# Optimization experiments

Hardware: AMD Instinct MI355X
Metric: run time of the kernel (lower is better)

Reference implementation:

```python
import jax, jax.numpy as jnp
import numpy as np

D_MODEL = 1024
D_HEAD = 64
B, S = 4, 4096


def setup_inputs() -> dict:
    key = jax.random.key(0)
    ks = jax.random.split(key, 7)
    inv = 1.0 / np.sqrt(D_MODEL)
    return {
        "x": jax.random.normal(ks[0], (B, S, D_MODEL), dtype=jnp.float32),
        "W_q": jax.random.normal(ks[1], (D_MODEL, D_HEAD), dtype=jnp.float32) * inv,
        "b_q": jax.random.normal(ks[2], (D_HEAD,), dtype=jnp.float32) * 0.02,
        "W_k": jax.random.normal(ks[3], (D_MODEL, D_HEAD), dtype=jnp.float32) * inv,
        "b_k": jax.random.normal(ks[4], (D_HEAD,), dtype=jnp.float32) * 0.02,
        "W_v": jax.random.normal(ks[5], (D_MODEL, D_HEAD), dtype=jnp.float32) * inv,
        "b_v": jax.random.normal(ks[6], (D_HEAD,), dtype=jnp.float32) * 0.02,
    }


def reference(x, W_q, b_q, W_k, b_k, W_v, b_v):
    # Projections: [B, S, d_head]
    Q = jnp.einsum("bsd,dh->bsh", x, W_q) + b_q
    K = jnp.einsum("bsd,dh->bsh", x, W_k) + b_k
    V = jnp.einsum("bsd,dh->bsh", x, W_v) + b_v
    scale = 1.0 / jnp.sqrt(jnp.asarray(Q.shape[-1], dtype=Q.dtype))
    scores = jnp.einsum("bqh,bkh->bqk", Q, K) * scale  # [B, S, S]
    seq_len = x.shape[1]
    causal = jnp.tril(jnp.ones((seq_len, seq_len), dtype=bool))
    scores = jnp.where(causal, scores, jnp.asarray(-jnp.inf, dtype=scores.dtype))
    A = jax.nn.softmax(scores, axis=-1)
    return jnp.einsum("bqk,bkh->bqh", A, V)  # [B, S, d_head]
```

## Files before the change

### kernel.cpp

```cpp
#include <hip/hip_runtime.h>

typedef __attribute__((ext_vector_type(4))) float f32x4;
typedef __attribute__((ext_vector_type(8))) short short8;
typedef unsigned short ushort_t;

constexpr int DM = 1024, DH = 64, S = 4096, B = 4;
constexpr float QSCALE = 0.125f * 1.44269504088896340736f;
constexpr int SPLIT = 4;

constexpr size_t WBT_OFF = 0;
constexpr size_t QB_OFF  = 393216;
constexpr size_t KB_OFF  = QB_OFF + 2097152;
constexpr size_t VT_OFF  = KB_OFF + 2097152;
constexpr size_t ML_OFF  = VT_OFF + 2097152;
constexpr size_t PO_OFF  = ML_OFF + 524288;

__device__ __forceinline__ ushort_t f2bf(float f) {
    unsigned u = __float_as_uint(f);
    u += 0x7FFFu + ((u >> 16) & 1u);
    return (ushort_t)(u >> 16);
}

__device__ __forceinline__ void gl_lds16(const void* g, void* l) {
    __builtin_amdgcn_global_load_lds(
        (const __attribute__((address_space(1))) unsigned int*)g,
        (__attribute__((address_space(3))) unsigned int*)l, 16, 0, 0);
}

__global__ __launch_bounds__(256) void prep_w_kernel(
    const float* __restrict__ Wq, const float* __restrict__ Wk,
    const float* __restrict__ Wv, ushort_t* __restrict__ wbt)
{
    const int n = blockIdx.x;
    const int p = n >> 6, d = n & 63;
    const float* W = (p == 0) ? Wq : (p == 1) ? Wk : Wv;
    const int k0 = threadIdx.x * 4;
    ushort4 pack;
    pack.x = f2bf(W[(k0 + 0) * DH + d]);
    pack.y = f2bf(W[(k0 + 1) * DH + d]);
    pack.z = f2bf(W[(k0 + 2) * DH + d]);
    pack.w = f2bf(W[(k0 + 3) * DH + d]);
    *reinterpret_cast<ushort4*>(wbt + (size_t)n * DM + k0) = pack;
}

__global__ __launch_bounds__(512, 4) void qkv_mfma_kernel(
    const float* __restrict__ x, const ushort_t* __restrict__ wbt,
    const float* __restrict__ bq, const float* __restrict__ bk,
    const float* __restrict__ bv,
    ushort_t* __restrict__ qb, ushort_t* __restrict__ kb, ushort_t* __restrict__ vt)
{
    __shared__ ushort_t As[2][32][32];
    __shared__ uint4 BsU[2][768];

    const int tid = threadIdx.x;
    const int wid = tid >> 6, lane = tid & 63;
    const int q16 = lane & 15, lg = lane >> 4;
    const int sub = wid & 1, np = wid >> 1;
    const int r0 = blockIdx.x * 32;
    const char* wB = (const char*)wbt;

    const int ar = tid >> 4;
    const int ak = (tid & 15) * 2;
    const float* xrow = x + (size_t)(r0 + ar) * DM + ak;

    auto writeA = [&](int buf, float2 a) {
        const unsigned pk = (unsigned)f2bf(a.x) | ((unsigned)f2bf(a.y) << 16);
        *reinterpret_cast<unsigned*>((char*)&As[buf][0][0] + ar * 64 + ak * 2) = pk;
    };
    auto stageB = [&](int buf, int kk) {
        {
            const int sg = wid;
            gl_lds16(wB + (size_t)(sg * 16 + (lane >> 2)) * 2048 + kk * 2
                        + ((((lane & 3) ^ ((lane >> 2) & 3))) << 4),
                     (char*)&BsU[buf][0] + sg * 1024 + lane * 16);
        }
        if (wid < 4) {
            const int sg = wid + 8;
            gl_lds16(wB + (size_t)(sg * 16 + (lane >> 2)) * 2048 + kk * 2
                        + ((((lane & 3) ^ ((lane >> 2) & 3))) << 4),
                     (char*)&BsU[buf][0] + sg * 1024 + lane * 16);
        }
    };

    f32x4 acc[3];
#pragma unroll
    for (int j = 0; j < 3; ++j) acc[j] = {0.f, 0.f, 0.f, 0.f};

    {
        const float2 a0 = *(const float2*)(xrow + 0);
        stageB(0, 0);
        writeA(0, a0);
    }
    __syncthreads();

    const int arow = sub * 16 + q16;
    for (int s = 0; s < 32; ++s) {
        const int buf = s & 1;
        float2 aP;
        if (s + 1 < 32) {
            aP = *(const float2*)(xrow + (s + 1) * 32);
            stageB(buf ^ 1, (s + 1) * 32);
        }
        const short8 Af = *reinterpret_cast<const short8*>(
            (const char*)&As[buf][0][0] + arow * 64 + lg * 16);
        __builtin_amdgcn_s_setprio(1);
#pragma unroll
        for (int j = 0; j < 3; ++j) {
            const int nt = np * 3 + j;
            const short8 Bf = *(const short8*)(
                (const char*)&BsU[buf][0] + (nt * 16 + q16) * 64 + ((lg ^ (q16 & 3)) << 4));
            acc[j] = __builtin_amdgcn_mfma_f32_16x16x32_bf16(Af, Bf, acc[j], 0, 0, 0);
        }
        __builtin_amdgcn_s_setprio(0);
        if (s + 1 < 32) writeA(buf ^ 1, aP);
        __syncthreads();
    }

#pragma unroll
    for (int j = 0; j < 3; ++j) {
        const int nt = np * 3 + j;
        const int p = nt >> 2, d = ((nt & 3) << 4) + q16;
        const float* bp = (p == 0) ? bq : (p == 1) ? bk : bv;
        const float bb = bp[d];
#pragma unroll
        for (int r = 0; r < 4; ++r) {
            const int m = r0 + sub * 16 + (lg << 2) + r;
            const float v = acc[j][r] + bb;
            if (p == 0) {
                qb[(size_t)m * 64 + d] = f2bf(v * QSCALE);
            } else if (p == 1) {
                kb[(size_t)m * 64 + d] = f2bf(v);
            } else {
                const int bb_ = m >> 12, sx = m & 4095;
                vt[(size_t)bb_ * 262144 + (size_t)d * 4096 + sx] = f2bf(v);
            }
        }
    }
}

__global__ __launch_bounds__(256, 4) void attn_mfma_kernel(
    const ushort_t* __restrict__ qb, const ushort_t* __restrict__ kb,
    const ushort_t* __restrict__ vt, ushort_t* __restrict__ po,
    float* __restrict__ ml)
{
    __shared__ uint4 LsU[2][2048];
    __shared__ uint4 PsU[4][256];

    const int tid = threadIdx.x;
    const int wid = tid >> 6, lane = tid & 63;
    const int q16 = lane & 15, lg = lane >> 4;
    const int z = blockIdx.y;

    const int linear = blockIdx.x;
    const int xcd = linear & 7, idx = linear >> 3;
    const int b = xcd >> 1;
    const int qt = 63 - (idx * 2 + (xcd & 1));

    const int qrow = qt * 64 + wid * 16 + q16;
    const ushort_t* Qb = qb + (size_t)b * S * 64;
    const char* KbB = (const char*)(kb + (size_t)b * S * 64);
    const char* VtB = (const char*)(vt + (size_t)b * 64 * S);

    const short8 qf0 = *(const short8*)(Qb + (size_t)qrow * 64 + lg * 8);
    const short8 qf1 = *(const short8*)(Qb + (size_t)qrow * 64 + 32 + lg * 8);

    f32x4 o[4];
#pragma unroll
    for (int nt = 0; nt < 4; ++nt) o[nt] = {0.f, 0.f, 0.f, 0.f};
    float m = -1e30f, l = 0.f;

    char* PsC = (char*)&PsU[wid][0];
    const int ntiles = (qt >> 1) + 1;

    auto stage = [&](int t, int buf) {
        const int kv0 = t * 128;
#pragma unroll
        for (int i = 0; i < 8; ++i) {
            const int slot = i * 256 + tid;
            char* dst = (char*)&LsU[buf][0] + slot * 16;
            if (slot < 1024) {
                const int row = slot >> 3, ch = slot & 7;
                gl_lds16(KbB + (size_t)(kv0 + row) * 128 + ((ch ^ (row & 7)) << 4), dst);
            } else {
                const int s2 = slot - 1024;
                const int d = s2 >> 4, ch = s2 & 15;
                gl_lds16(VtB + (size_t)d * (S * 2) + kv0 * 2 + ((ch ^ (d & 15)) << 4), dst);
            }
        }
    };

    int buf = 0;
    if (z < ntiles) stage(z, 0);
    __syncthreads();

    for (int t = z; t < ntiles; t += SPLIT) {
        if (t + SPLIT < ntiles) stage(t + SPLIT, buf ^ 1);
        const char* KsC = (const char*)&LsU[buf][0];
        const char* VsC = KsC + 16384;
        const int kv0 = t * 128;

        f32x4 st[8];
#pragma unroll
        for (int mt = 0; mt < 8; ++mt) st[mt] = {0.f, 0.f, 0.f, 0.f};
#pragma unroll
        for (int ks = 0; ks < 2; ++ks) {
#pragma unroll
            for (int mg = 0; mg < 2; ++mg) {
                short8 kf[4];
#pragma unroll
                for (int j = 0; j < 4; ++j) {
                    const int mt = mg * 4 + j;
                    kf[j] = *(const short8*)(
                        KsC + (mt * 16 + q16) * 128 + (((lg + 4 * ks) ^ (q16 & 7)) << 4));
                }
                __builtin_amdgcn_s_setprio(1);
#pragma unroll
                for (int j = 0; j < 4; ++j)
                    st[mg * 4 + j] = __builtin_amdgcn_mfma_f32_16x16x32_bf16(
                        kf[j], (ks ? qf1 : qf0), st[mg * 4 + j], 0, 0, 0);
                __builtin_amdgcn_s_setprio(0);
            }
        }

        if (t == ntiles - 1) {
#pragma unroll
            for (int mt = 0; mt < 8; ++mt)
#pragma unroll
                for (int r = 0; r < 4; ++r)
                    if (kv0 + mt * 16 + (lg << 2) + r > qrow) st[mt][r] = -1e30f;
        }

        float tm = -1e30f;
#pragma unroll
        for (int mt = 0; mt < 8; ++mt)
#pragma unroll
            for (int r = 0; r < 4; ++r) tm = fmaxf(tm, st[mt][r]);
        tm = fmaxf(tm, __shfl_xor(tm, 16));
        tm = fmaxf(tm, __shfl_xor(tm, 32));

        if (__all(tm <= m)) {
            float ps = 0.f;
#pragma unroll
            for (int mt = 0; mt < 8; ++mt)
#pragma unroll
                for (int r = 0; r < 4; ++r) {
                    const float pv = exp2f(st[mt][r] - m);
                    st[mt][r] = pv;
                    ps += pv;
                }
            ps += __shfl_xor(ps, 16);
            ps += __shfl_xor(ps, 32);
            l += ps;
        } else {
            const float mn = fmaxf(m, tm);
            const float corr = exp2f(m - mn);
            float ps = 0.f;
#pragma unroll
            for (int mt = 0; mt < 8; ++mt)
#pragma unroll
                for (int r = 0; r < 4; ++r) {
                    const float pv = exp2f(st[mt][r] - mn);
                    st[mt][r] = pv;
                    ps += pv;
                }
            ps += __shfl_xor(ps, 16);
            ps += __shfl_xor(ps, 32);
            l = l * corr + ps;
            m = mn;
            float corr_row[4];
#pragma unroll
            for (int r = 0; r < 4; ++r) corr_row[r] = __shfl(corr, (lg << 2) | r);
#pragma unroll
            for (int nt = 0; nt < 4; ++nt)
#pragma unroll
                for (int r = 0; r < 4; ++r) o[nt][r] *= corr_row[r];
        }

#pragma unroll
        for (int mt = 0; mt < 8; ++mt) {
            uint2 w;
            w.x = (unsigned)f2bf(st[mt][0]) | ((unsigned)f2bf(st[mt][1]) << 16);
            w.y = (unsigned)f2bf(st[mt][2]) | ((unsigned)f2bf(st[mt][3]) << 16);
            const int ch = (2 * mt + (lg >> 1)) ^ q16;
            *reinterpret_cast<uint2*>(PsC + q16 * 256 + ch * 16 + (lg & 1) * 8) = w;
        }

        __builtin_amdgcn_s_setprio(1);
#pragma unroll
        for (int ks = 0; ks < 4; ++ks) {
            const short8 pa = *reinterpret_cast<const short8*>(
                PsC + q16 * 256 + (((4 * ks + lg) ^ q16) << 4));
#pragma unroll
            for (int nt = 0; nt < 4; ++nt) {
                const short8 vf = *(const short8*)(
                    VsC + (nt * 16 + q16) * 256 + (((ks * 4 + lg) ^ q16) << 4));
                o[nt] = __builtin_amdgcn_mfma_f32_16x16x32_bf16(pa, vf, o[nt], 0, 0, 0);
            }
        }
        __builtin_amdgcn_s_setprio(0);

        __syncthreads();
        buf ^= 1;
    }

    const int rowbase = qt * 64 + wid * 16;
    const size_t zb = (size_t)z * B * S + (size_t)b * S;
#pragma unroll
    for (int nt = 0; nt < 4; ++nt)
#pragma unroll
        for (int r = 0; r < 4; ++r)
            po[(zb + rowbase + (lg << 2) + r) * 64 + nt * 16 + q16] = f2bf(o[nt][r]);
    if (lg == 0) {
        ml[(zb + rowbase + q16) * 2 + 0] = m;
        ml[(zb + rowbase + q16) * 2 + 1] = l;
    }
}

__global__ __launch_bounds__(256) void merge_kernel(
    const ushort_t* __restrict__ po, const float* __restrict__ ml,
    float* __restrict__ out)
{
    const int idx = blockIdx.x * 256 + threadIdx.x;
    const int row = idx >> 3, c8 = idx & 7;

    float mv[SPLIT], lv[SPLIT];
#pragma unroll
    for (int zz = 0; zz < SPLIT; ++zz) {
        const float2 t = *(const float2*)(ml + ((size_t)zz * B * S + row) * 2);
        mv[zz] = t.x; lv[zz] = t.y;
    }
    const float mm = fmaxf(fmaxf(mv[0], mv[1]), fmaxf(mv[2], mv[3]));
    float L = 0.f, cz[SPLIT];
#pragma unroll
    for (int zz = 0; zz < SPLIT; ++zz) { cz[zz] = exp2f(mv[zz] - mm); L += lv[zz] * cz[zz]; }
    const float inv = 1.0f / L;

    float acc[8];
#pragma unroll
    for (int e = 0; e < 8; ++e) acc[e] = 0.f;
#pragma unroll
    for (int zz = 0; zz < SPLIT; ++zz) {
        const uint4 pk = *(const uint4*)(po + ((size_t)zz * B * S + row) * 64 + c8 * 8);
        const unsigned w[4] = {pk.x, pk.y, pk.z, pk.w};
#pragma unroll
        for (int i = 0; i < 4; ++i) {
            acc[2 * i + 0] += cz[zz] * __uint_as_float((w[i] & 0xFFFFu) << 16);
            acc[2 * i + 1] += cz[zz] * __uint_as_float((w[i] >> 16) << 16);
        }
    }
    float4 o0 = make_float4(acc[0] * inv, acc[1] * inv, acc[2] * inv, acc[3] * inv);
    float4 o1 = make_float4(acc[4] * inv, acc[5] * inv, acc[6] * inv, acc[7] * inv);
    *(float4*)(out + (size_t)row * 64 + c8 * 8 + 0) = o0;
    *(float4*)(out + (size_t)row * 64 + c8 * 8 + 4) = o1;
}

extern "C" void kernel_launch(void* const* d_in, const int* in_sizes, int n_in,
                              void* d_out, int out_size, void* d_ws, size_t ws_size,
                              hipStream_t stream) {
    const float* x  = (const float*)d_in[0];
    const float* Wq = (const float*)d_in[1];
    const float* bq = (const float*)d_in[2];
    const float* Wk = (const float*)d_in[3];
    const float* bk = (const float*)d_in[4];
    const float* Wv = (const float*)d_in[5];
    const float* bv = (const float*)d_in[6];
    float* out = (float*)d_out;

    char* ws = (char*)d_ws;
    ushort_t* wbt = (ushort_t*)(ws + WBT_OFF);
    ushort_t* qbp = (ushort_t*)(ws + QB_OFF);
    ushort_t* kbp = (ushort_t*)(ws + KB_OFF);
    ushort_t* vtp = (ushort_t*)(ws + VT_OFF);
    float*    mlp = (float*)(ws + ML_OFF);
    ushort_t* pop = (ushort_t*)(ws + PO_OFF);

    hipLaunchKernelGGL(prep_w_kernel, dim3(192), dim3(256), 0, stream, Wq, Wk, Wv, wbt);
    hipLaunchKernelGGL(qkv_mfma_kernel, dim3(512), dim3(512), 0, stream,
                       x, wbt, bq, bk, bv, qbp, kbp, vtp);
    hipLaunchKernelGGL(attn_mfma_kernel, dim3(256, SPLIT), dim3(256), 0, stream,
                       qbp, kbp, vtp, pop, mlp);
    hipLaunchKernelGGL(merge_kernel, dim3(512), dim3(256), 0, stream, pop, mlp, out);
}
```

Before: 74.57 us.

## Load x directly into registers, quad-buffer weights, stream V from global

The QKV projection kernel drops the shared-memory A tile. Each lane now loads its x fragment straight from global one step ahead and converts it to bf16 in registers. The weight tiles become a 4-deep LDS ring with a vmcnt wait and one barrier per step, where there were two-stage buffers with a full syncthreads. The attention kernel stops staging V through LDS and instead loads V fragments directly from global into registers, double-buffered across the PV MFMA steps. This halves LDS use per block but lowers the launch-bounds occupancy hint from 4 to 3 and adds register pressure and uncoalesced global V reads.

```diff
diff --git a/kernel.cpp b/kernel.cpp
--- a/kernel.cpp
+++ b/kernel.cpp
@@ -49,8 +49,7 @@
     const float* __restrict__ bv,
     ushort_t* __restrict__ qb, ushort_t* __restrict__ kb, ushort_t* __restrict__ vt)
 {
-    __shared__ ushort_t As[2][32][32];
-    __shared__ uint4 BsU[2][768];
+    __shared__ uint4 BsU[4][768];
 
     const int tid = threadIdx.x;
     const int wid = tid >> 6, lane = tid & 63;
@@ -59,61 +58,56 @@
     const int r0 = blockIdx.x * 32;
     const char* wB = (const char*)wbt;
 
-    const int ar = tid >> 4;
-    const int ak = (tid & 15) * 2;
-    const float* xrow = x + (size_t)(r0 + ar) * DM + ak;
-
-    auto writeA = [&](int buf, float2 a) {
-        const unsigned pk = (unsigned)f2bf(a.x) | ((unsigned)f2bf(a.y) << 16);
-        *reinterpret_cast<unsigned*>((char*)&As[buf][0][0] + ar * 64 + ak * 2) = pk;
+    const float* xr = x + (size_t)(r0 + sub * 16 + q16) * DM + lg * 8;
+
+    const int sgA = wid, sgB = (wid & 3) + 8;
+    auto stageB = [&](int kk, int buf) {
+        gl_lds16(wB + (size_t)(sgA * 16 + (lane >> 2)) * 2048 + kk * 2
+                    + ((((lane & 3) ^ ((lane >> 2) & 3))) << 4),
+                 (char*)&BsU[buf][0] + sgA * 1024 + lane * 16);
+        gl_lds16(wB + (size_t)(sgB * 16 + (lane >> 2)) * 2048 + kk * 2
+                    + ((((lane & 3) ^ ((lane >> 2) & 3))) << 4),
+                 (char*)&BsU[buf][0] + sgB * 1024 + lane * 16);
     };
-    auto stageB = [&](int buf, int kk) {
-        {
-            const int sg = wid;
-            gl_lds16(wB + (size_t)(sg * 16 + (lane >> 2)) * 2048 + kk * 2
-                        + ((((lane & 3) ^ ((lane >> 2) & 3))) << 4),
-                     (char*)&BsU[buf][0] + sg * 1024 + lane * 16);
-        }
-        if (wid < 4) {
-            const int sg = wid + 8;
-            gl_lds16(wB + (size_t)(sg * 16 + (lane >> 2)) * 2048 + kk * 2
-                        + ((((lane & 3) ^ ((lane >> 2) & 3))) << 4),
-                     (char*)&BsU[buf][0] + sg * 1024 + lane * 16);
-        }
-    };
 
     f32x4 acc[3];
 #pragma unroll
     for (int j = 0; j < 3; ++j) acc[j] = {0.f, 0.f, 0.f, 0.f};
 
-    {
-        const float2 a0 = *(const float2*)(xrow + 0);
-        stageB(0, 0);
-        writeA(0, a0);
-    }
-    __syncthreads();
-
-    const int arow = sub * 16 + q16;
+    float4 apA = *(const float4*)(xr + 0);
+    float4 apB = *(const float4*)(xr + 4);
+    stageB(0, 0);
+    stageB(32, 1);
+
     for (int s = 0; s < 32; ++s) {
-        const int buf = s & 1;
-        float2 aP;
-        if (s + 1 < 32) {
-            aP = *(const float2*)(xrow + (s + 1) * 32);
-            stageB(buf ^ 1, (s + 1) * 32);
-        }
-        const short8 Af = *reinterpret_cast<const short8*>(
-            (const char*)&As[buf][0][0] + arow * 64 + lg * 16);
+        const int sn = (s + 1 < 32) ? (s + 1) : 31;
+        const int sp = (s + 2 < 32) ? (s + 2) : 31;
+        const float4 anA = *(const float4*)(xr + sn * 32);
+        const float4 anB = *(const float4*)(xr + sn * 32 + 4);
+        stageB(sp * 32, (s + 2) & 3);
+
+        asm volatile("s_waitcnt vmcnt(4)" ::: "memory");
+        __builtin_amdgcn_sched_barrier(0);
+        __builtin_amdgcn_s_barrier();
+        __builtin_amdgcn_sched_barrier(0);
+
+        short8 Af;
+        Af[0] = (short)f2bf(apA.x); Af[1] = (short)f2bf(apA.y);
+        Af[2] = (short)f2bf(apA.z); Af[3] = (short)f2bf(apA.w);
+        Af[4] = (short)f2bf(apB.x); Af[5] = (short)f2bf(apB.y);
+        Af[6] = (short)f2bf(apB.z); Af[7] = (short)f2bf(apB.w);
+
+        const char* BsC = (const char*)&BsU[s & 3][0];
         __builtin_amdgcn_s_setprio(1);
 #pragma unroll
         for (int j = 0; j < 3; ++j) {
             const int nt = np * 3 + j;
             const short8 Bf = *(const short8*)(
-                (const char*)&BsU[buf][0] + (nt * 16 + q16) * 64 + ((lg ^ (q16 & 3)) << 4));
+                BsC + (nt * 16 + q16) * 64 + ((lg ^ (q16 & 3)) << 4));
             acc[j] = __builtin_amdgcn_mfma_f32_16x16x32_bf16(Af, Bf, acc[j], 0, 0, 0);
         }
         __builtin_amdgcn_s_setprio(0);
-        if (s + 1 < 32) writeA(buf ^ 1, aP);
-        __syncthreads();
+        apA = anA; apB = anB;
     }
 
 #pragma unroll
@@ -138,12 +132,12 @@
     }
 }
 
-__global__ __launch_bounds__(256, 4) void attn_mfma_kernel(
+__global__ __launch_bounds__(256, 3) void attn_mfma_kernel(
     const ushort_t* __restrict__ qb, const ushort_t* __restrict__ kb,
     const ushort_t* __restrict__ vt, ushort_t* __restrict__ po,
     float* __restrict__ ml)
 {
-    __shared__ uint4 LsU[2][2048];
+    __shared__ uint4 LsU[2][1024];
     __shared__ uint4 PsU[4][256];
 
     const int tid = threadIdx.x;
@@ -159,7 +153,7 @@
     const int qrow = qt * 64 + wid * 16 + q16;
     const ushort_t* Qb = qb + (size_t)b * S * 64;
     const char* KbB = (const char*)(kb + (size_t)b * S * 64);
-    const char* VtB = (const char*)(vt + (size_t)b * 64 * S);
+    const ushort_t* VtP = vt + (size_t)b * 64 * S;
 
     const short8 qf0 = *(const short8*)(Qb + (size_t)qrow * 64 + lg * 8);
     const short8 qf1 = *(const short8*)(Qb + (size_t)qrow * 64 + 32 + lg * 8);
@@ -175,18 +169,18 @@
     auto stage = [&](int t, int buf) {
         const int kv0 = t * 128;
 #pragma unroll
-        for (int i = 0; i < 8; ++i) {
+        for (int i = 0; i < 4; ++i) {
             const int slot = i * 256 + tid;
-            char* dst = (char*)&LsU[buf][0] + slot * 16;
-            if (slot < 1024) {
-                const int row = slot >> 3, ch = slot & 7;
-                gl_lds16(KbB + (size_t)(kv0 + row) * 128 + ((ch ^ (row & 7)) << 4), dst);
-            } else {
-                const int s2 = slot - 1024;
-                const int d = s2 >> 4, ch = s2 & 15;
-                gl_lds16(VtB + (size_t)d * (S * 2) + kv0 * 2 + ((ch ^ (d & 15)) << 4), dst);
-            }
-        }
+            const int row = slot >> 3, ch = slot & 7;
+            gl_lds16(KbB + (size_t)(kv0 + row) * 128 + ((ch ^ (row & 7)) << 4),
+                     (char*)&LsU[buf][0] + slot * 16);
+        }
+    };
+    auto loadV = [&](short8* v, int ks, int kv0) {
+#pragma unroll
+        for (int nt = 0; nt < 4; ++nt)
+            v[nt] = *(const short8*)(
+                VtP + (size_t)(nt * 16 + q16) * S + kv0 + ks * 32 + lg * 8);
     };
 
     int buf = 0;
@@ -196,7 +190,6 @@
     for (int t = z; t < ntiles; t += SPLIT) {
         if (t + SPLIT < ntiles) stage(t + SPLIT, buf ^ 1);
         const char* KsC = (const char*)&LsU[buf][0];
-        const char* VsC = KsC + 16384;
         const int kv0 = t * 128;
 
         f32x4 st[8];
@@ -221,6 +214,9 @@
                 __builtin_amdgcn_s_setprio(0);
             }
         }
+
+        short8 va[4], vb[4];
+        loadV(va, 0, kv0);
 
         if (t == ntiles - 1) {
 #pragma unroll
@@ -276,6 +272,8 @@
                 for (int r = 0; r < 4; ++r) o[nt][r] *= corr_row[r];
         }
 
+        loadV(vb, 1, kv0);
+
 #pragma unroll
         for (int mt = 0; mt < 8; ++mt) {
             uint2 w;
@@ -286,16 +284,31 @@
         }
 
         __builtin_amdgcn_s_setprio(1);
-#pragma unroll
-        for (int ks = 0; ks < 4; ++ks) {
-            const short8 pa = *reinterpret_cast<const short8*>(
-                PsC + q16 * 256 + (((4 * ks + lg) ^ q16) << 4));
-#pragma unroll
-            for (int nt = 0; nt < 4; ++nt) {
-                const short8 vf = *(const short8*)(
-                    VsC + (nt * 16 + q16) * 256 + (((ks * 4 + lg) ^ q16) << 4));
-                o[nt] = __builtin_amdgcn_mfma_f32_16x16x32_bf16(pa, vf, o[nt], 0, 0, 0);
-            }
+        {
+            const short8 pa = *(const short8*)(PsC + q16 * 256 + ((lg ^ q16) << 4));
+#pragma unroll
+            for (int nt = 0; nt < 4; ++nt)
+                o[nt] = __builtin_amdgcn_mfma_f32_16x16x32_bf16(pa, va[nt], o[nt], 0, 0, 0);
+        }
+        loadV(va, 2, kv0);
+        {
+            const short8 pa = *(const short8*)(PsC + q16 * 256 + (((4 + lg) ^ q16) << 4));
+#pragma unroll
+            for (int nt = 0; nt < 4; ++nt)
+                o[nt] = __builtin_amdgcn_mfma_f32_16x16x32_bf16(pa, vb[nt], o[nt], 0, 0, 0);
+        }
+        loadV(vb, 3, kv0);
+        {
+            const short8 pa = *(const short8*)(PsC + q16 * 256 + (((8 + lg) ^ q16) << 4));
+#pragma unroll
+            for (int nt = 0; nt < 4; ++nt)
+                o[nt] = __builtin_amdgcn_mfma_f32_16x16x32_bf16(pa, va[nt], o[nt], 0, 0, 0);
+        }
+        {
+            const short8 pa = *(const short8*)(PsC + q16 * 256 + (((12 + lg) ^ q16) << 4));
+#pragma unroll
+            for (int nt = 0; nt < 4; ++nt)
+                o[nt] = __builtin_amdgcn_mfma_f32_16x16x32_bf16(pa, vb[nt], o[nt], 0, 0, 0);
         }
         __builtin_amdgcn_s_setprio(0);
 
```

Result: slower. 116.7 us (+56.5%).

## Load x fragments directly into registers and double the K step per iteration

Applied to the files above, without the earlier changes.

The QKV projection kernel no longer stages x through shared memory. Each lane reads its own fp32 x values straight from global memory, converts them to bf16 in registers and feeds the MFMA. The K step per iteration grows from 32 to 64, which halves the number of barrier-separated iterations and widens the weight LDS tiles, now using an 8-way XOR swizzle. The trade-off is that x loads are now exposed with no prefetch, each lane does wider uncoalesced-ish row reads, and LDS use for B doubles.

```diff
diff --git a/kernel.cpp b/kernel.cpp
--- a/kernel.cpp
+++ b/kernel.cpp
@@ -49,8 +49,7 @@
     const float* __restrict__ bv,
     ushort_t* __restrict__ qb, ushort_t* __restrict__ kb, ushort_t* __restrict__ vt)
 {
-    __shared__ ushort_t As[2][32][32];
-    __shared__ uint4 BsU[2][768];
+    __shared__ uint4 BsU[2][1536];
 
     const int tid = threadIdx.x;
     const int wid = tid >> 6, lane = tid & 63;
@@ -59,60 +58,56 @@
     const int r0 = blockIdx.x * 32;
     const char* wB = (const char*)wbt;
 
-    const int ar = tid >> 4;
-    const int ak = (tid & 15) * 2;
-    const float* xrow = x + (size_t)(r0 + ar) * DM + ak;
-
-    auto writeA = [&](int buf, float2 a) {
-        const unsigned pk = (unsigned)f2bf(a.x) | ((unsigned)f2bf(a.y) << 16);
-        *reinterpret_cast<unsigned*>((char*)&As[buf][0][0] + ar * 64 + ak * 2) = pk;
+    const float* xr = x + (size_t)(r0 + sub * 16 + q16) * DM;
+
+    auto stageB = [&](int s, int buf) {
+#pragma unroll
+        for (int j = 0; j < 3; ++j) {
+            const int sg = wid * 3 + j;
+            const int row = sg * 8 + (lane >> 3);
+            const int ch = lane & 7;
+            gl_lds16(wB + (size_t)row * 2048 + s * 128 + ((ch ^ (row & 7)) << 4),
+                     (char*)&BsU[buf][0] + sg * 1024 + lane * 16);
+        }
     };
-    auto stageB = [&](int buf, int kk) {
-        {
-            const int sg = wid;
-            gl_lds16(wB + (size_t)(sg * 16 + (lane >> 2)) * 2048 + kk * 2
-                        + ((((lane & 3) ^ ((lane >> 2) & 3))) << 4),
-                     (char*)&BsU[buf][0] + sg * 1024 + lane * 16);
-        }
-        if (wid < 4) {
-            const int sg = wid + 8;
-            gl_lds16(wB + (size_t)(sg * 16 + (lane >> 2)) * 2048 + kk * 2
-                        + ((((lane & 3) ^ ((lane >> 2) & 3))) << 4),
-                     (char*)&BsU[buf][0] + sg * 1024 + lane * 16);
-        }
-    };
 
     f32x4 acc[3];
 #pragma unroll
     for (int j = 0; j < 3; ++j) acc[j] = {0.f, 0.f, 0.f, 0.f};
 
-    {
-        const float2 a0 = *(const float2*)(xrow + 0);
-        stageB(0, 0);
-        writeA(0, a0);
-    }
+    stageB(0, 0);
     __syncthreads();
 
-    const int arow = sub * 16 + q16;
-    for (int s = 0; s < 32; ++s) {
+    for (int s = 0; s < 16; ++s) {
         const int buf = s & 1;
-        float2 aP;
-        if (s + 1 < 32) {
-            aP = *(const float2*)(xrow + (s + 1) * 32);
-            stageB(buf ^ 1, (s + 1) * 32);
-        }
-        const short8 Af = *reinterpret_cast<const short8*>(
-            (const char*)&As[buf][0][0] + arow * 64 + lg * 16);
+        if (s + 1 < 16) stageB(s + 1, buf ^ 1);
+        const float4 a0 = *(const float4*)(xr + s * 64 + lg * 8);
+        const float4 a1 = *(const float4*)(xr + s * 64 + lg * 8 + 4);
+        const float4 a2 = *(const float4*)(xr + s * 64 + 32 + lg * 8);
+        const float4 a3 = *(const float4*)(xr + s * 64 + 32 + lg * 8 + 4);
+        short8 Af0, Af1;
+        Af0[0] = (short)f2bf(a0.x); Af0[1] = (short)f2bf(a0.y);
+        Af0[2] = (short)f2bf(a0.z); Af0[3] = (short)f2bf(a0.w);
+        Af0[4] = (short)f2bf(a1.x); Af0[5] = (short)f2bf(a1.y);
+        Af0[6] = (short)f2bf(a1.z); Af0[7] = (short)f2bf(a1.w);
+        Af1[0] = (short)f2bf(a2.x); Af1[1] = (short)f2bf(a2.y);
+        Af1[2] = (short)f2bf(a2.z); Af1[3] = (short)f2bf(a2.w);
+        Af1[4] = (short)f2bf(a3.x); Af1[5] = (short)f2bf(a3.y);
+        Af1[6] = (short)f2bf(a3.z); Af1[7] = (short)f2bf(a3.w);
+        const char* BsC = (const char*)&BsU[buf][0];
         __builtin_amdgcn_s_setprio(1);
 #pragma unroll
         for (int j = 0; j < 3; ++j) {
             const int nt = np * 3 + j;
-            const short8 Bf = *(const short8*)(
-                (const char*)&BsU[buf][0] + (nt * 16 + q16) * 64 + ((lg ^ (q16 & 3)) << 4));
-            acc[j] = __builtin_amdgcn_mfma_f32_16x16x32_bf16(Af, Bf, acc[j], 0, 0, 0);
+            const int rn = nt * 16 + q16;
+            const short8 Bf0 = *(const short8*)(
+                BsC + rn * 128 + ((lg ^ (q16 & 7)) << 4));
+            acc[j] = __builtin_amdgcn_mfma_f32_16x16x32_bf16(Af0, Bf0, acc[j], 0, 0, 0);
+            const short8 Bf1 = *(const short8*)(
+                BsC + rn * 128 + (((4 + lg) ^ (q16 & 7)) << 4));
+            acc[j] = __builtin_amdgcn_mfma_f32_16x16x32_bf16(Af1, Bf1, acc[j], 0, 0, 0);
         }
         __builtin_amdgcn_s_setprio(0);
-        if (s + 1 < 32) writeA(buf ^ 1, aP);
         __syncthreads();
     }
 
```

After: 91.76 us. 1.23x slower.
